# Performance work log

Hardware: AMD Instinct MI355X
Metric: run time of the kernel (lower is better)

The kernel has to match this reference:

```python
import jax, jax.numpy as jnp
import numpy as np

N, E, D_IN, H, DH = 50000, 800000, 128, 4, 32
NEG_SLOPE = 0.01  # torch nn.LeakyReLU() default
EPS = 1e-16       # torch_geometric softmax epsilon


def setup_inputs() -> dict:
    key = jax.random.key(0)
    k0, k1, k2, k3, k4 = jax.random.split(key, 5)
    x = jax.random.normal(k0, (N, D_IN), dtype=jnp.float32)
    edge_index = jax.random.randint(k1, (2, E), 0, N, dtype=jnp.int64)
    # Glorot-uniform-ish scales
    s_proj = (6.0 / (D_IN + H * DH)) ** 0.5
    W_proj = jax.random.uniform(k2, (D_IN, H * DH), jnp.float32, -s_proj, s_proj)
    s_att = (6.0 / (H + 2 * DH)) ** 0.5
    att_w = jax.random.uniform(k3, (H, 2 * DH), jnp.float32, -s_att, s_att)
    W_skip = jax.random.uniform(k4, (D_IN, H * DH), jnp.float32, -s_proj, s_proj)
    return {"x": x, "W_proj": W_proj, "att_w": att_w, "W_skip": W_skip,
            "edge_index": edge_index}


def reference(x, W_proj, att_w, W_skip, edge_index):
    num_nodes = x.shape[0]
    h = (x @ W_proj).reshape(num_nodes, H, DH)          # [N,H,Dh]
    src, dst = edge_index[0], edge_index[1]
    h_src = h[src]                                      # [E,H,Dh] gather
    h_dst = h[dst]                                      # [E,H,Dh] gather
    # einsum('nah,nah->na', cat([h_src,h_dst],-1), a) == split-a form:
    a_src, a_dst = att_w[:, :DH], att_w[:, DH:]
    e = (jnp.einsum('ehd,hd->eh', h_src, a_src)
         + jnp.einsum('ehd,hd->eh', h_dst, a_dst))      # [E,H]
    e = jax.nn.leaky_relu(e, NEG_SLOPE)
    # segment softmax grouped by dst (max-stabilized, as in torch_geometric)
    e_max = jax.ops.segment_max(e, dst, num_segments=num_nodes)  # [N,H]
    e_exp = jnp.exp(e - e_max[dst])
    denom = jax.ops.segment_sum(e_exp, dst, num_segments=num_nodes)
    alpha = e_exp / (denom[dst] + EPS)                  # [E,H]
    # scatter-add aggregation (index_add_ by dst)
    h_prime = jax.ops.segment_sum(alpha[..., None] * h_src, dst,
                                  num_segments=num_nodes)  # [N,H,Dh]
    h_prime = h_prime + (x @ W_skip).reshape(num_nodes, H, DH)
    return h_prime.reshape(num_nodes, H * DH)
```

## Files before the change

### kernel.cpp

```cpp
#include <hip/hip_runtime.h>
#include <hip/hip_bf16.h>

#define N_NODES 50000
#define E_EDGES 800000
#define NHEAD 4
#define DHEAD 32
#define DOUT 128
#define NEG_SLOPE 0.01f
#define EPS_F 1e-16f
#define DMAX 256
#define ELP 264
#define NB 196
#define CAP 8192
#define XSP 136
#define NGB 782

typedef __attribute__((ext_vector_type(8))) short bf16x8;
typedef __attribute__((ext_vector_type(4))) float f32x4;

__device__ __forceinline__ float bf2f(unsigned short u) {
    return __uint_as_float((unsigned)u << 16);
}
__device__ __forceinline__ unsigned short f2bf(float f) {
    return __bfloat16_as_ushort(__float2bfloat16(f));
}

__device__ __forceinline__ void load_edge(const int* __restrict__ ei, int isI64,
                                          int e, int& src, int& dst) {
    if (isI64) { src = ei[2 * e]; dst = ei[2 * (E_EDGES + e)]; }
    else       { src = ei[e];     dst = ei[E_EDGES + e]; }
}

__global__ __launch_bounds__(128) void k_prep(const float* __restrict__ Wp,
                                              const float* __restrict__ Ws,
                                              const int* __restrict__ ei,
                                              unsigned short* __restrict__ Wt,
                                              int* __restrict__ bucketCnt,
                                              int* __restrict__ flag) {
    int b = blockIdx.x;
    if (b < 256) {
        int c = b, k = threadIdx.x;
        float v = (c < DOUT) ? Wp[k * DOUT + c] : Ws[k * DOUT + (c - DOUT)];
        int nf = c >> 4, cl = c & 15;
        int ks = k >> 5, r = k & 31, lq = r >> 3, e = r & 7;
        Wt[(((nf * 4 + ks) << 6) + lq * 16 + cl) * 8 + e] = f2bf(v);
    } else {
        __shared__ int cnt;
        if (threadIdx.x == 0) cnt = 0;
        if (threadIdx.x < 128 && (int)threadIdx.x < NB) {
            bucketCnt[threadIdx.x] = 0;
            if (threadIdx.x + 128 < NB) bucketCnt[threadIdx.x + 128] = 0;
        }
        __syncthreads();
        int nz = 0;
        #pragma unroll
        for (int k2 = 0; k2 < 16; ++k2) {
            int pos = (threadIdx.x + k2 * 128) * 2 + 1;
            if (ei[pos] != 0) nz = 1;
        }
        if (nz) atomicOr(&cnt, 1);
        __syncthreads();
        if (threadIdx.x == 0) *flag = (cnt == 0) ? 1 : 0;
    }
}

__global__ __launch_bounds__(256) void k_gemm_part(const float* __restrict__ x,
                                                   const unsigned short* __restrict__ Wt,
                                                   const float* __restrict__ att,
                                                   const int* __restrict__ ei,
                                                   const int* __restrict__ flag,
                                                   int* __restrict__ bucketCnt,
                                                   unsigned* __restrict__ payload,
                                                   unsigned short* __restrict__ hb,
                                                   float* __restrict__ as_,
                                                   float* __restrict__ ad_,
                                                   float* __restrict__ out) {
    __shared__ __align__(16) char BUF[64 * XSP * 2];
    const int tid = threadIdx.x;

    if (blockIdx.x < 256) {
        int* hist = (int*)BUF;
        int* curs = hist + NB;
        const int base = blockIdx.x * 3125;
        const int isI64 = *flag;

        for (int i = tid; i < NB; i += 256) hist[i] = 0;
        __syncthreads();
        for (int i = tid; i < 3125; i += 256) {
            int src, dst;
            load_edge(ei, isI64, base + i, src, dst);
            if ((unsigned)dst < N_NODES) atomicAdd(&hist[dst >> 8], 1);
        }
        __syncthreads();
        for (int i = tid; i < NB; i += 256)
            curs[i] = atomicAdd(&bucketCnt[i], hist[i]);
        __syncthreads();
        for (int i = tid; i < 3125; i += 256) {
            int src, dst;
            load_edge(ei, isI64, base + i, src, dst);
            if ((unsigned)src >= N_NODES || (unsigned)dst >= N_NODES) continue;
            int b = dst >> 8;
            int pos = atomicAdd(&curs[b], 1);
            if (pos < CAP)
                payload[((size_t)b << 13) + pos] = ((unsigned)(dst & 255) << 16) | (unsigned)src;
        }
        return;
    }

    unsigned short* XSB = (unsigned short*)BUF;
    const int gbp  = blockIdx.x - 256;
    const int gb   = gbp >> 1;
    const int half = gbp & 1;
    const int rw  = tid >> 6;
    const int l   = tid & 63;
    const int l15 = l & 15;
    const int lq  = l >> 4;
    const int rowbase = gb * 64 + rw * 16;

    {
        #pragma unroll
        for (int it = 0; it < 8; ++it) {
            int e = it * 1024 + tid * 4;
            int row = e >> 7, col = e & 127;
            int grow = gb * 64 + row;
            if (grow > N_NODES - 1) grow = N_NODES - 1;
            float4 v = *(const float4*)(x + (size_t)grow * DOUT + col);
            ushort4 pk = make_ushort4(f2bf(v.x), f2bf(v.y), f2bf(v.z), f2bf(v.w));
            *(ushort4*)(XSB + row * XSP + col) = pk;
        }
    }
    __syncthreads();

    bf16x8 xfr[4];
    const char* xrow = (const char*)XSB + (rw * 16 + l15) * (XSP * 2);
    #pragma unroll
    for (int ks = 0; ks < 4; ++ks)
        xfr[ks] = *(const bf16x8*)(xrow + ks * 64 + lq * 16);

    f32x4 acc[8];
    #pragma unroll
    for (int nf = 0; nf < 8; ++nf) acc[nf] = (f32x4)(0.0f);

    const int nfbase = half * 8;
    #pragma unroll
    for (int nf = 0; nf < 8; ++nf) {
        #pragma unroll
        for (int ks = 0; ks < 4; ++ks) {
            bf16x8 w = *(const bf16x8*)(Wt + (((((nfbase + nf) * 4 + ks) << 6) + l) << 3));
            acc[nf] = __builtin_amdgcn_mfma_f32_16x16x32_bf16(w, xfr[ks], acc[nf], 0, 0, 0);
        }
    }

    const int r = rowbase + l15;
    if (half == 0) {
        float ps1[4] = {0.f, 0.f, 0.f, 0.f}, ps2[4] = {0.f, 0.f, 0.f, 0.f};
        #pragma unroll
        for (int nf = 0; nf < 8; ++nf) {
            int hd = nf >> 1;
            int jb = (nf & 1) * 16 + lq * 4;
            float4 w1 = *(const float4*)(att + hd * 2 * DHEAD + jb);
            float4 w2 = *(const float4*)(att + hd * 2 * DHEAD + DHEAD + jb);
            f32x4 v = acc[nf];
            ps1[hd] += v[0] * w1.x + v[1] * w1.y + v[2] * w1.z + v[3] * w1.w;
            ps2[hd] += v[0] * w2.x + v[1] * w2.y + v[2] * w2.z + v[3] * w2.w;
            ushort4 pk = make_ushort4(f2bf(v[0]), f2bf(v[1]), f2bf(v[2]), f2bf(v[3]));
            *(ushort4*)(hb + (size_t)r * DOUT + nf * 16 + lq * 4) = pk;
        }
        #pragma unroll
        for (int hd = 0; hd < 4; ++hd) {
            ps1[hd] += __shfl_xor(ps1[hd], 16); ps1[hd] += __shfl_xor(ps1[hd], 32);
            ps2[hd] += __shfl_xor(ps2[hd], 16); ps2[hd] += __shfl_xor(ps2[hd], 32);
        }
        if (lq == 0) {
            #pragma unroll
            for (int hd = 0; hd < 4; ++hd) {
                as_[(size_t)r * 4 + hd] = ps1[hd];
                ad_[(size_t)r * 4 + hd] = ps2[hd];
            }
        }
    } else {
        if (r < N_NODES) {
            #pragma unroll
            for (int nf = 0; nf < 8; ++nf) {
                f32x4 v = acc[nf];
                *(float4*)(out + (size_t)r * DOUT + nf * 16 + lq * 4) =
                    make_float4(v[0], v[1], v[2], v[3]);
            }
        }
    }
}

__global__ __launch_bounds__(256) void k_csr(const int* __restrict__ bucketCnt,
                                             const unsigned* __restrict__ payload,
                                             int* __restrict__ deg,
                                             int* __restrict__ ofs,
                                             int* __restrict__ srcs) {
    __shared__ int h[256];
    __shared__ int cur[256];
    __shared__ int sc[256];
    const int b = blockIdx.x;
    const int t = threadIdx.x;
    int cnt = bucketCnt[b];
    if (cnt > CAP) cnt = CAP;
    const unsigned* __restrict__ pl = payload + ((size_t)b << 13);

    h[t] = 0;
    __syncthreads();
    for (int i = t; i < cnt; i += 256) atomicAdd(&h[pl[i] >> 16], 1);
    __syncthreads();
    int v = h[t];
    sc[t] = v;
    __syncthreads();
    #pragma unroll
    for (int off = 1; off < 256; off <<= 1) {
        int u = (t >= off) ? sc[t - off] : 0;
        __syncthreads();
        sc[t] += u;
        __syncthreads();
    }
    int ex = sc[t] - v;
    cur[t] = ex;
    int n = (b << 8) + t;
    if (n < N_NODES) { deg[n] = v; ofs[n] = (b << 13) + ex; }
    __syncthreads();
    for (int i = t; i < cnt; i += 256) {
        unsigned p = pl[i];
        int pos = atomicAdd(&cur[p >> 16], 1);
        srcs[((size_t)b << 13) + pos] = (int)(p & 0xFFFFu);
    }
}

__global__ __launch_bounds__(128) void k_gat(const int* __restrict__ ofs,
                                             const int* __restrict__ deg,
                                             const int* __restrict__ srcs,
                                             const float* __restrict__ as_,
                                             const float* __restrict__ ad_,
                                             const unsigned short* __restrict__ hb,
                                             float* __restrict__ out) {
    __shared__ float EL[2][NHEAD * ELP];
    __shared__ int   SRC[2][DMAX];

    const int sub = threadIdx.x >> 6;
    const int k   = threadIdx.x & 63;
    const int hd  = k >> 4;
    const int l16 = k & 15;
    const int n = blockIdx.x * 2 + sub;
    const int o = ofs[n];
    const int d = deg[n];
    const unsigned* __restrict__ hbu = (const unsigned*)hb;
    float* ELn = EL[sub];
    int*   SRCn = SRC[sub];

    int fast = __syncthreads_and(d <= DMAX);

    if (fast) {
        const float4 adv4 = *(const float4*)(ad_ + (size_t)n * 4);
        for (int e = k; e < d; e += 64) {
            int s = srcs[o + e];
            SRCn[e] = s;
            float4 a4 = *(const float4*)(as_ + (size_t)s * 4);
            float e0 = a4.x + adv4.x, e1 = a4.y + adv4.y;
            float e2 = a4.z + adv4.z, e3 = a4.w + adv4.w;
            ELn[0 * ELP + e] = (e0 > 0.0f) ? e0 : NEG_SLOPE * e0;
            ELn[1 * ELP + e] = (e1 > 0.0f) ? e1 : NEG_SLOPE * e1;
            ELn[2 * ELP + e] = (e2 > 0.0f) ? e2 : NEG_SLOPE * e2;
            ELn[3 * ELP + e] = (e3 > 0.0f) ? e3 : NEG_SLOPE * e3;
        }
        __syncthreads();
        float m = -3.4e38f;
        for (int i = l16; i < d; i += 16) m = fmaxf(m, ELn[hd * ELP + i]);
        #pragma unroll
        for (int off = 8; off; off >>= 1) m = fmaxf(m, __shfl_xor(m, off));
        float den = 0.0f;
        for (int i = l16; i < d; i += 16) {
            float p = __expf(ELn[hd * ELP + i] - m);
            ELn[hd * ELP + i] = p;
            den += p;
        }
        #pragma unroll
        for (int off = 8; off; off >>= 1) den += __shfl_xor(den, off);
        __syncthreads();
        float num0 = 0.0f, num1 = 0.0f;
        int i = 0;
        for (; i + 4 <= d; i += 4) {
            int s0 = SRCn[i], s1 = SRCn[i + 1], s2 = SRCn[i + 2], s3 = SRCn[i + 3];
            unsigned u0 = hbu[(size_t)s0 * (DOUT / 2) + k];
            unsigned u1 = hbu[(size_t)s1 * (DOUT / 2) + k];
            unsigned u2 = hbu[(size_t)s2 * (DOUT / 2) + k];
            unsigned u3 = hbu[(size_t)s3 * (DOUT / 2) + k];
            float p0 = ELn[hd * ELP + i];
            float p1 = ELn[hd * ELP + i + 1];
            float p2 = ELn[hd * ELP + i + 2];
            float p3 = ELn[hd * ELP + i + 3];
            num0 = fmaf(p0, bf2f((unsigned short)(u0 & 0xffff)), num0);
            num1 = fmaf(p0, bf2f((unsigned short)(u0 >> 16)), num1);
            num0 = fmaf(p1, bf2f((unsigned short)(u1 & 0xffff)), num0);
            num1 = fmaf(p1, bf2f((unsigned short)(u1 >> 16)), num1);
            num0 = fmaf(p2, bf2f((unsigned short)(u2 & 0xffff)), num0);
            num1 = fmaf(p2, bf2f((unsigned short)(u2 >> 16)), num1);
            num0 = fmaf(p3, bf2f((unsigned short)(u3 & 0xffff)), num0);
            num1 = fmaf(p3, bf2f((unsigned short)(u3 >> 16)), num1);
        }
        for (; i < d; ++i) {
            float p = ELn[hd * ELP + i];
            int s = SRCn[i];
            unsigned u = hbu[(size_t)s * (DOUT / 2) + k];
            num0 = fmaf(p, bf2f((unsigned short)(u & 0xffff)), num0);
            num1 = fmaf(p, bf2f((unsigned short)(u >> 16)), num1);
        }
        float inv = 1.0f / (den + EPS_F);
        float2* op = (float2*)(out + (size_t)n * DOUT + 2 * k);
        float2 sk = *op;
        *op = make_float2(num0 * inv + sk.x, num1 * inv + sk.y);
    } else {
        const float adv = ad_[(size_t)n * 4 + hd];
        float m = -3.4e38f;
        for (int i = 0; i < d; ++i) {
            float el = as_[(size_t)srcs[o + i] * 4 + hd] + adv;
            el = (el > 0.0f) ? el : NEG_SLOPE * el;
            m = fmaxf(m, el);
        }
        float den = 0.0f, num0 = 0.0f, num1 = 0.0f;
        for (int i = 0; i < d; ++i) {
            int s = srcs[o + i];
            float el = as_[(size_t)s * 4 + hd] + adv;
            el = (el > 0.0f) ? el : NEG_SLOPE * el;
            float p = __expf(el - m);
            den += p;
            unsigned u = hbu[(size_t)s * (DOUT / 2) + k];
            num0 = fmaf(p, bf2f((unsigned short)(u & 0xffff)), num0);
            num1 = fmaf(p, bf2f((unsigned short)(u >> 16)), num1);
        }
        float inv = 1.0f / (den + EPS_F);
        float2* op = (float2*)(out + (size_t)n * DOUT + 2 * k);
        float2 sk = *op;
        *op = make_float2(num0 * inv + sk.x, num1 * inv + sk.y);
    }
}

extern "C" void kernel_launch(void* const* d_in, const int* in_sizes, int n_in,
                              void* d_out, int out_size, void* d_ws, size_t ws_size,
                              hipStream_t stream) {
    const float* x   = (const float*)d_in[0];
    const float* Wp  = (const float*)d_in[1];
    const float* att = (const float*)d_in[2];
    const float* Ws  = (const float*)d_in[3];
    const int*   ei  = (const int*)d_in[4];
    float* out = (float*)d_out;

    char* ws = (char*)d_ws;
    unsigned short* hb        = (unsigned short*)(ws);
    unsigned short* Wt        = (unsigned short*)(ws + 12812288);
    float*          as_       = (float*)(ws + 12877824);
    float*          ad_       = (float*)(ws + 13678592);
    int*            deg       = (int*)(ws + 14479360);
    int*            ofs       = (int*)(ws + 14680064);
    unsigned*       payload   = (unsigned*)(ws + 14880768);
    int*            srcs      = (int*)(ws + 21303296);
    int*            bucketCnt = (int*)(ws + 27725824);
    int*            flag      = (int*)(ws + 27726848);

    k_prep<<<257, 128, 0, stream>>>(Wp, Ws, ei, Wt, bucketCnt, flag);
    k_gemm_part<<<256 + 2 * NGB, 256, 0, stream>>>(
        x, Wt, att, ei, flag, bucketCnt, payload, hb, as_, ad_, out);
    k_csr<<<NB, 256, 0, stream>>>(bucketCnt, payload, deg, ofs, srcs);
    k_gat<<<N_NODES / 2, 128, 0, stream>>>(ofs, deg, srcs, as_, ad_, hb, out);
}
```

Measured before the change: 99.41 us.

## Split GAT aggregation by head and parallelize edges across lane groups

The aggregation kernel is restructured so that each block handles one head for four destination nodes, one wave per node. Within a wave, four lane groups process different edges at once, and the partial sums are combined with shuffles. The softmax is computed per head with full-wave reductions and pre-normalized alphas. This raises memory-level parallelism on the neighbour gathers, at the cost of repeating the index and score loads for each head and issuing narrower 64-byte gathers.

Result: slower. 175.6 us (+76.7%).

```diff
diff --git a/kernel.cpp b/kernel.cpp
--- a/kernel.cpp
+++ b/kernel.cpp
@@ -9,7 +9,6 @@
 #define NEG_SLOPE 0.01f
 #define EPS_F 1e-16f
 #define DMAX 256
-#define ELP 264
 #define NB 196
 #define CAP 8192
 #define XSP 136
@@ -230,111 +229,107 @@
     }
 }
 
-__global__ __launch_bounds__(128) void k_gat(const int* __restrict__ ofs,
+__global__ __launch_bounds__(256) void k_gat(const int* __restrict__ ofs,
                                              const int* __restrict__ deg,
                                              const int* __restrict__ srcs,
                                              const float* __restrict__ as_,
                                              const float* __restrict__ ad_,
                                              const unsigned short* __restrict__ hb,
                                              float* __restrict__ out) {
-    __shared__ float EL[2][NHEAD * ELP];
-    __shared__ int   SRC[2][DMAX];
-
-    const int sub = threadIdx.x >> 6;
-    const int k   = threadIdx.x & 63;
-    const int hd  = k >> 4;
-    const int l16 = k & 15;
-    const int n = blockIdx.x * 2 + sub;
+    __shared__ int   SRC[4][DMAX];
+    __shared__ float EL[4][DMAX];
+
+    const int hd  = blockIdx.x & 3;
+    const int bq  = blockIdx.x >> 2;
+    const int wid = threadIdx.x >> 6;
+    const int l   = threadIdx.x & 63;
+    const int g   = l >> 4;
+    const int c   = l & 15;
+    const int n   = bq * 4 + wid;
     const int o = ofs[n];
     const int d = deg[n];
     const unsigned* __restrict__ hbu = (const unsigned*)hb;
-    float* ELn = EL[sub];
-    int*   SRCn = SRC[sub];
+    int*   SRCw = SRC[wid];
+    float* ELw  = EL[wid];
 
     int fast = __syncthreads_and(d <= DMAX);
 
     if (fast) {
-        const float4 adv4 = *(const float4*)(ad_ + (size_t)n * 4);
-        for (int e = k; e < d; e += 64) {
-            int s = srcs[o + e];
-            SRCn[e] = s;
-            float4 a4 = *(const float4*)(as_ + (size_t)s * 4);
-            float e0 = a4.x + adv4.x, e1 = a4.y + adv4.y;
-            float e2 = a4.z + adv4.z, e3 = a4.w + adv4.w;
-            ELn[0 * ELP + e] = (e0 > 0.0f) ? e0 : NEG_SLOPE * e0;
-            ELn[1 * ELP + e] = (e1 > 0.0f) ? e1 : NEG_SLOPE * e1;
-            ELn[2 * ELP + e] = (e2 > 0.0f) ? e2 : NEG_SLOPE * e2;
-            ELn[3 * ELP + e] = (e3 > 0.0f) ? e3 : NEG_SLOPE * e3;
+        const float adv = ad_[(size_t)n * 4 + hd];
+        for (int i = l; i < d; i += 64) {
+            int s = srcs[o + i];
+            SRCw[i] = s;
+            float e = as_[(size_t)s * 4 + hd] + adv;
+            ELw[i] = (e > 0.0f) ? e : NEG_SLOPE * e;
         }
         __syncthreads();
         float m = -3.4e38f;
-        for (int i = l16; i < d; i += 16) m = fmaxf(m, ELn[hd * ELP + i]);
-        #pragma unroll
-        for (int off = 8; off; off >>= 1) m = fmaxf(m, __shfl_xor(m, off));
+        for (int i = l; i < d; i += 64) m = fmaxf(m, ELw[i]);
+        #pragma unroll
+        for (int off = 32; off; off >>= 1) m = fmaxf(m, __shfl_xor(m, off));
         float den = 0.0f;
-        for (int i = l16; i < d; i += 16) {
-            float p = __expf(ELn[hd * ELP + i] - m);
-            ELn[hd * ELP + i] = p;
+        for (int i = l; i < d; i += 64) {
+            float p = __expf(ELw[i] - m);
+            ELw[i] = p;
             den += p;
         }
         #pragma unroll
-        for (int off = 8; off; off >>= 1) den += __shfl_xor(den, off);
+        for (int off = 32; off; off >>= 1) den += __shfl_xor(den, off);
+        float inv = 1.0f / (den + EPS_F);
+        for (int i = l; i < d; i += 64) ELw[i] *= inv;
         __syncthreads();
         float num0 = 0.0f, num1 = 0.0f;
-        int i = 0;
-        for (; i + 4 <= d; i += 4) {
-            int s0 = SRCn[i], s1 = SRCn[i + 1], s2 = SRCn[i + 2], s3 = SRCn[i + 3];
-            unsigned u0 = hbu[(size_t)s0 * (DOUT / 2) + k];
-            unsigned u1 = hbu[(size_t)s1 * (DOUT / 2) + k];
-            unsigned u2 = hbu[(size_t)s2 * (DOUT / 2) + k];
-            unsigned u3 = hbu[(size_t)s3 * (DOUT / 2) + k];
-            float p0 = ELn[hd * ELP + i];
-            float p1 = ELn[hd * ELP + i + 1];
-            float p2 = ELn[hd * ELP + i + 2];
-            float p3 = ELn[hd * ELP + i + 3];
-            num0 = fmaf(p0, bf2f((unsigned short)(u0 & 0xffff)), num0);
-            num1 = fmaf(p0, bf2f((unsigned short)(u0 >> 16)), num1);
-            num0 = fmaf(p1, bf2f((unsigned short)(u1 & 0xffff)), num0);
-            num1 = fmaf(p1, bf2f((unsigned short)(u1 >> 16)), num1);
-            num0 = fmaf(p2, bf2f((unsigned short)(u2 & 0xffff)), num0);
-            num1 = fmaf(p2, bf2f((unsigned short)(u2 >> 16)), num1);
-            num0 = fmaf(p3, bf2f((unsigned short)(u3 & 0xffff)), num0);
-            num1 = fmaf(p3, bf2f((unsigned short)(u3 >> 16)), num1);
-        }
-        for (; i < d; ++i) {
-            float p = ELn[hd * ELP + i];
-            int s = SRCn[i];
-            unsigned u = hbu[(size_t)s * (DOUT / 2) + k];
-            num0 = fmaf(p, bf2f((unsigned short)(u & 0xffff)), num0);
-            num1 = fmaf(p, bf2f((unsigned short)(u >> 16)), num1);
-        }
-        float inv = 1.0f / (den + EPS_F);
-        float2* op = (float2*)(out + (size_t)n * DOUT + 2 * k);
-        float2 sk = *op;
-        *op = make_float2(num0 * inv + sk.x, num1 * inv + sk.y);
+        for (int i = 0; i < d; i += 4) {
+            int e = i + g;
+            if (e < d) {
+                float a = ELw[e];
+                unsigned u = hbu[(size_t)SRCw[e] * (DOUT / 2) + hd * 16 + c];
+                num0 = fmaf(a, bf2f((unsigned short)(u & 0xffff)), num0);
+                num1 = fmaf(a, bf2f((unsigned short)(u >> 16)), num1);
+            }
+        }
+        num0 += __shfl_xor(num0, 16); num0 += __shfl_xor(num0, 32);
+        num1 += __shfl_xor(num1, 16); num1 += __shfl_xor(num1, 32);
+        if (g == 0) {
+            float2* op = (float2*)(out + (size_t)n * DOUT + hd * DHEAD + 2 * c);
+            float2 sk = *op;
+            *op = make_float2(num0 + sk.x, num1 + sk.y);
+        }
     } else {
         const float adv = ad_[(size_t)n * 4 + hd];
         float m = -3.4e38f;
         for (int i = 0; i < d; ++i) {
-            float el = as_[(size_t)srcs[o + i] * 4 + hd] + adv;
-            el = (el > 0.0f) ? el : NEG_SLOPE * el;
-            m = fmaxf(m, el);
-        }
-        float den = 0.0f, num0 = 0.0f, num1 = 0.0f;
+            float e = as_[(size_t)srcs[o + i] * 4 + hd] + adv;
+            e = (e > 0.0f) ? e : NEG_SLOPE * e;
+            m = fmaxf(m, e);
+        }
+        float den = 0.0f;
         for (int i = 0; i < d; ++i) {
-            int s = srcs[o + i];
-            float el = as_[(size_t)s * 4 + hd] + adv;
-            el = (el > 0.0f) ? el : NEG_SLOPE * el;
-            float p = __expf(el - m);
-            den += p;
-            unsigned u = hbu[(size_t)s * (DOUT / 2) + k];
-            num0 = fmaf(p, bf2f((unsigned short)(u & 0xffff)), num0);
-            num1 = fmaf(p, bf2f((unsigned short)(u >> 16)), num1);
+            float e = as_[(size_t)srcs[o + i] * 4 + hd] + adv;
+            e = (e > 0.0f) ? e : NEG_SLOPE * e;
+            den += __expf(e - m);
         }
         float inv = 1.0f / (den + EPS_F);
-        float2* op = (float2*)(out + (size_t)n * DOUT + 2 * k);
-        float2 sk = *op;
-        *op = make_float2(num0 * inv + sk.x, num1 * inv + sk.y);
+        float num0 = 0.0f, num1 = 0.0f;
+        for (int i = 0; i < d; i += 4) {
+            int e = i + g;
+            if (e < d) {
+                int s = srcs[o + e];
+                float el = as_[(size_t)s * 4 + hd] + adv;
+                el = (el > 0.0f) ? el : NEG_SLOPE * el;
+                float a = __expf(el - m) * inv;
+                unsigned u = hbu[(size_t)s * (DOUT / 2) + hd * 16 + c];
+                num0 = fmaf(a, bf2f((unsigned short)(u & 0xffff)), num0);
+                num1 = fmaf(a, bf2f((unsigned short)(u >> 16)), num1);
+            }
+        }
+        num0 += __shfl_xor(num0, 16); num0 += __shfl_xor(num0, 32);
+        num1 += __shfl_xor(num1, 16); num1 += __shfl_xor(num1, 32);
+        if (g == 0) {
+            float2* op = (float2*)(out + (size_t)n * DOUT + hd * DHEAD + 2 * c);
+            float2 sk = *op;
+            *op = make_float2(num0 + sk.x, num1 + sk.y);
+        }
     }
 }
 
@@ -364,5 +359,5 @@
     k_gemm_part<<<256 + 2 * NGB, 256, 0, stream>>>(
         x, Wt, att, ei, flag, bucketCnt, payload, hb, as_, ad_, out);
     k_csr<<<NB, 256, 0, stream>>>(bucketCnt, payload, deg, ofs, srcs);
-    k_gat<<<N_NODES / 2, 128, 0, stream>>>(ofs, deg, srcs, as_, ad_, hb, out);
-}
+    k_gat<<<(N_NODES / 4) * 4, 256, 0, stream>>>(ofs, deg, srcs, as_, ad_, hb, out);
+}
```
